# Performance work log

Measured on AMD Instinct MI355X. Metric: run time of the kernel, lower is better.

## Reference

```python
import jax, jax.numpy as jnp
import numpy as np

BATCH, FIELDS, DIM = 1024, 39, 32
L0_OUT, L1_OUT = 256, 128  # cin_layer_size


def setup_inputs() -> dict:
    key = jax.random.key(0)
    ks = jax.random.split(key, 5)
    x = jax.random.normal(ks[0], (BATCH, FIELDS, DIM), dtype=jnp.float32)
    # Conv1d(kernel_size=1) weights stored as (out_channels, in_channels)
    w0 = jax.random.normal(ks[1], (L0_OUT, FIELDS * FIELDS), dtype=jnp.float32) * 0.02
    b0 = jax.random.normal(ks[2], (L0_OUT,), dtype=jnp.float32) * 0.02
    w1 = jax.random.normal(ks[3], (L1_OUT, FIELDS * (L0_OUT // 2)), dtype=jnp.float32) * 0.02
    b1 = jax.random.normal(ks[4], (L1_OUT,), dtype=jnp.float32) * 0.02
    return {"x": x, "w0": w0, "b0": b0, "w1": w1, "b1": b1}


def _cin_layer(x0, h_prev, w, b):
    # outer product over field axes at each embedding position, then 1x1 conv (= GEMM over channels)
    bsz, m, d = x0.shape
    z = jnp.einsum('bmd,bnd->bmnd', x0, h_prev).reshape(bsz, m * h_prev.shape[1], d)
    return jax.nn.relu(jnp.einsum('bid,oi->bod', z, w) + b[None, :, None])


def reference(x, w0, b0, w1, b1):
    # Layer 0: cross x with itself -> (B, m*m, D) -> conv -> relu
    h0 = _cin_layer(x, x, w0, b0)            # (B, 256, D)
    h1a, h1b = jnp.split(h0, 2, axis=1)      # each (B, 128, D); h1a feeds next layer
    # Layer 1 (final): cross x with h1a
    h1 = _cin_layer(x, h1a, w1, b1)          # (B, 128, D)
    # sum-pool over embedding dim of concatenated hidden outputs (hidden_layer[1:])
    return jnp.sum(jnp.concatenate([h1b, h1], axis=1), axis=-1)  # (B, 256)
```

## Files before the change

### kernel.cpp

```cpp
#include <hip/hip_runtime.h>


typedef __bf16 bf16x8 __attribute__((ext_vector_type(8)));
typedef float f32x4 __attribute__((ext_vector_type(4)));

#define NB 2
#define NBLK 512
#define THREADS 256
#define K0STEPS 50

__global__ __launch_bounds__(256) void prep_kernel(
    const float* __restrict__ w0, const float* __restrict__ w1,
    __bf16* __restrict__ w0b, __bf16* __restrict__ w1p) {
  int stride = gridDim.x * blockDim.x;
  int tid = blockIdx.x * blockDim.x + threadIdx.x;
  const int n0 = K0STEPS * 256 * 32;
  for (int idx = tid; idx < n0; idx += stride) {
    int j = idx & 31, o = (idx >> 5) & 255, blk = idx >> 13;
    int ip = blk * 32 + j;
    float v = 0.f;
    if (ip < 1560) {
      unsigned m = (unsigned)ip / 40u;
      unsigned n = (unsigned)ip - m * 40u;
      if (n < 39u) v = w0[o * 1521 + m * 39 + n];
    }
    w0b[idx] = (__bf16)v;
  }
  const int n1 = 39 * 4 * 128 * 32;
  for (int idx = tid; idx < n1; idx += stride) {
    int j = idx & 31, o = (idx >> 5) & 127, q = idx >> 12;
    int ks = q & 3, m = q >> 2;
    w1p[idx] = (__bf16)w1[o * 4992 + m * 128 + ks * 32 + j];
  }
}

__global__ __launch_bounds__(256, 2) void cin_kernel(
    const float* __restrict__ x,
    const __bf16* __restrict__ w0b, const float* __restrict__ b0,
    const __bf16* __restrict__ w1p, const float* __restrict__ b1,
    float* __restrict__ out) {
  __shared__ __align__(16) __bf16 xs[NB * 32 * 40];
  __shared__ __align__(16) __bf16 zsm[2 * 64 * 32];
  __shared__ __align__(16) __bf16 h1[NB * 32 * 136];

  const int t = threadIdx.x;
  const int bb = blockIdx.x * NB;
  const int w = t >> 6;
  const int l15 = t & 15;
  const int lhi = (t >> 4) & 3;
  const int col = t & 63;
  const int kg = t >> 6;
  const int zwoff = col * 32 + ((kg ^ ((col >> 1) & 3)) * 8);

  for (int idx = t; idx < NB * 39 * 32; idx += THREADS) {
    int b = idx / 1248; int rem = idx - b * 1248;
    int m = rem >> 5; int d = rem & 31;
    xs[(b * 32 + d) * 40 + m] = (__bf16)x[(bb + b) * 1248 + rem];
  }
  if (t < NB * 32) xs[t * 40 + 39] = (__bf16)0.f;
  __syncthreads();

  int boff[4];
#pragma unroll
  for (int nt = 0; nt < 4; ++nt) {
    int cc = nt * 16 + l15;
    boff[nt] = cc * 32 + ((lhi ^ ((cc >> 1) & 3)) * 8);
  }

  f32x4 acc[4][4] = {};

  auto loadA0 = [&](int s, bf16x8 (&af)[4]) {
#pragma unroll
    for (int mt = 0; mt < 4; ++mt) {
      int o = w * 64 + mt * 16 + l15;
      af[mt] = *(const bf16x8*)(w0b + s * 8192 + o * 32 + lhi * 8);
    }
  };
  auto zgen0 = [&](int s, int buf) {
    int i0 = s * 32 + kg * 8;
    unsigned m = (unsigned)i0 / 40u;
    unsigned nb = (unsigned)i0 - m * 40u;
    float xm = (float)xs[col * 40 + m];
    bf16x8 xn = *(const bf16x8*)&xs[col * 40 + nb];
    bf16x8 vz;
#pragma unroll
    for (int jj = 0; jj < 8; ++jj) vz[jj] = (__bf16)(xm * (float)xn[jj]);
    *(bf16x8*)&zsm[buf * 2048 + zwoff] = vz;
  };
  auto compute0 = [&](int buf, bf16x8 (&af)[4]) {
    bf16x8 bfr[4];
#pragma unroll
    for (int nt = 0; nt < 4; ++nt) bfr[nt] = *(const bf16x8*)&zsm[buf * 2048 + boff[nt]];
#pragma unroll
    for (int mt = 0; mt < 4; ++mt)
#pragma unroll
      for (int nt = 0; nt < 4; ++nt)
        acc[mt][nt] = __builtin_amdgcn_mfma_f32_16x16x32_bf16(af[mt], bfr[nt], acc[mt][nt], 0, 0, 0);
  };

  bf16x8 afA[4], afB[4];
  loadA0(0, afA);
  zgen0(0, 0);
  __syncthreads();
  for (int s = 0; s < K0STEPS; s += 2) {
    loadA0(s + 1, afB);
    zgen0(s + 1, 1);
    compute0(0, afA);
    __syncthreads();
    if (s + 2 < K0STEPS) { loadA0(s + 2, afA); zgen0(s + 2, 0); }
    compute0(1, afB);
    __syncthreads();
  }

  if (w < 2) {
#pragma unroll
    for (int mt = 0; mt < 4; ++mt) {
#pragma unroll
      for (int nt = 0; nt < 4; ++nt) {
        int c = nt * 16 + l15;
        int hbase = c * 136;
#pragma unroll
        for (int r = 0; r < 4; ++r) {
          int o = w * 64 + mt * 16 + lhi * 4 + r;
          float v = fmaxf(acc[mt][nt][r] + b0[o], 0.f);
          h1[hbase + o] = (__bf16)v;
        }
      }
    }
  } else {
#pragma unroll
    for (int mt = 0; mt < 4; ++mt) {
#pragma unroll
      for (int r = 0; r < 4; ++r) {
        int o = w * 64 + mt * 16 + lhi * 4 + r;
        float bias = b0[o];
        float sb0 = 0.f, sb1 = 0.f;
#pragma unroll
        for (int nt = 0; nt < 4; ++nt) {
          float v = fmaxf(acc[mt][nt][r] + bias, 0.f);
          v += __shfl_xor(v, 1); v += __shfl_xor(v, 2);
          v += __shfl_xor(v, 4); v += __shfl_xor(v, 8);
          if (nt < 2) sb0 += v; else sb1 += v;
        }
        if (l15 == 0) {
          out[(bb + 0) * 256 + (o - 128)] = sb0;
          out[(bb + 1) * 256 + (o - 128)] = sb1;
        }
      }
    }
  }
  __syncthreads();

  bf16x8 hf[4][4];
#pragma unroll
  for (int ks = 0; ks < 4; ++ks)
#pragma unroll
    for (int nt = 0; nt < 4; ++nt)
      hf[ks][nt] = *(const bf16x8*)&h1[(nt * 16 + l15) * 136 + ks * 32 + lhi * 8];

  f32x4 acc2[2][4] = {};

  auto loadA1 = [&](int m, bf16x8 (&wf)[4][2]) {
#pragma unroll
    for (int ks = 0; ks < 4; ++ks)
#pragma unroll
      for (int mt = 0; mt < 2; ++mt) {
        int o = w * 32 + mt * 16 + l15;
        wf[ks][mt] = *(const bf16x8*)(w1p + ((m * 4 + ks) * 128 + o) * 32 + lhi * 8);
      }
  };
  auto computeM = [&](int m, bf16x8 (&wf)[4][2]) {
    float xmv[4];
#pragma unroll
    for (int nt = 0; nt < 4; ++nt) xmv[nt] = (float)xs[(nt * 16 + l15) * 40 + m];
    f32x4 Y[2][4];
#pragma unroll
    for (int ks = 0; ks < 4; ++ks)
#pragma unroll
      for (int mt = 0; mt < 2; ++mt)
#pragma unroll
        for (int nt = 0; nt < 4; ++nt) {
          f32x4 cin = (ks == 0) ? (f32x4){0.f, 0.f, 0.f, 0.f} : Y[mt][nt];
          Y[mt][nt] = __builtin_amdgcn_mfma_f32_16x16x32_bf16(wf[ks][mt], hf[ks][nt], cin, 0, 0, 0);
        }
#pragma unroll
    for (int mt = 0; mt < 2; ++mt)
#pragma unroll
      for (int nt = 0; nt < 4; ++nt)
#pragma unroll
        for (int r = 0; r < 4; ++r)
          acc2[mt][nt][r] += xmv[nt] * Y[mt][nt][r];
  };

  bf16x8 wfA[4][2], wfB[4][2];
  loadA1(0, wfA);
  loadA1(1, wfB);
  for (int m = 0; m < 38; m += 2) {
    computeM(m, wfA);
    if (m + 2 < 39) loadA1(m + 2, wfA);
    computeM(m + 1, wfB);
    if (m + 3 < 39) loadA1(m + 3, wfB);
  }
  computeM(38, wfA);

#pragma unroll
  for (int mt = 0; mt < 2; ++mt) {
#pragma unroll
    for (int r = 0; r < 4; ++r) {
      int o = w * 32 + mt * 16 + lhi * 4 + r;
      float bias = b1[o];
      float sb0 = 0.f, sb1 = 0.f;
#pragma unroll
      for (int nt = 0; nt < 4; ++nt) {
        float v = fmaxf(acc2[mt][nt][r] + bias, 0.f);
        v += __shfl_xor(v, 1); v += __shfl_xor(v, 2);
        v += __shfl_xor(v, 4); v += __shfl_xor(v, 8);
        if (nt < 2) sb0 += v; else sb1 += v;
      }
      if (l15 == 0) {
        out[(bb + 0) * 256 + 128 + o] = sb0;
        out[(bb + 1) * 256 + 128 + o] = sb1;
      }
    }
  }
}

extern "C" void kernel_launch(void* const* d_in, const int* in_sizes, int n_in,
                              void* d_out, int out_size, void* d_ws, size_t ws_size,
                              hipStream_t stream) {
  const float* x  = (const float*)d_in[0];
  const float* w0 = (const float*)d_in[1];
  const float* b0 = (const float*)d_in[2];
  const float* w1 = (const float*)d_in[3];
  const float* b1 = (const float*)d_in[4];
  float* out = (float*)d_out;

  __bf16* w0b = (__bf16*)d_ws;
  __bf16* w1p = w0b + K0STEPS * 256 * 32;

  prep_kernel<<<256, 256, 0, stream>>>(w0, w1, w0b, w1p);
  cin_kernel<<<NBLK, THREADS, 0, stream>>>(x, w0b, b0, w1p, b1, out);
}
```

Before: 104.7 us.

## Generate layer-0 Z fragments in registers per wave, dropping shared staging and barriers

Layer 0 of the CIN kernel no longer stages the outer-product Z tile in a double-buffered shared-memory array. Each wave now builds its own MFMA B fragments directly from xs in registers, which removes the per-step LDS writes and reads and both __syncthreads per iteration. The cost is that all four waves recompute the same Z values, roughly four times the conversion and multiply work per block. The division by 40 is also replaced with a multiply-shift, and the weight prefetch now runs two steps ahead.

```diff
diff --git a/kernel.cpp b/kernel.cpp
--- a/kernel.cpp
+++ b/kernel.cpp
@@ -40,7 +40,6 @@
     const __bf16* __restrict__ w1p, const float* __restrict__ b1,
     float* __restrict__ out) {
   __shared__ __align__(16) __bf16 xs[NB * 32 * 40];
-  __shared__ __align__(16) __bf16 zsm[2 * 64 * 32];
   __shared__ __align__(16) __bf16 h1[NB * 32 * 136];
 
   const int t = threadIdx.x;
@@ -48,9 +47,6 @@
   const int w = t >> 6;
   const int l15 = t & 15;
   const int lhi = (t >> 4) & 3;
-  const int col = t & 63;
-  const int kg = t >> 6;
-  const int zwoff = col * 32 + ((kg ^ ((col >> 1) & 3)) * 8);
 
   for (int idx = t; idx < NB * 39 * 32; idx += THREADS) {
     int b = idx / 1248; int rem = idx - b * 1248;
@@ -60,13 +56,6 @@
   if (t < NB * 32) xs[t * 40 + 39] = (__bf16)0.f;
   __syncthreads();
 
-  int boff[4];
-#pragma unroll
-  for (int nt = 0; nt < 4; ++nt) {
-    int cc = nt * 16 + l15;
-    boff[nt] = cc * 32 + ((lhi ^ ((cc >> 1) & 3)) * 8);
-  }
-
   f32x4 acc[4][4] = {};
 
   auto loadA0 = [&](int s, bf16x8 (&af)[4]) {
@@ -76,40 +65,40 @@
       af[mt] = *(const bf16x8*)(w0b + s * 8192 + o * 32 + lhi * 8);
     }
   };
-  auto zgen0 = [&](int s, int buf) {
-    int i0 = s * 32 + kg * 8;
-    unsigned m = (unsigned)i0 / 40u;
-    unsigned nb = (unsigned)i0 - m * 40u;
-    float xm = (float)xs[col * 40 + m];
-    bf16x8 xn = *(const bf16x8*)&xs[col * 40 + nb];
-    bf16x8 vz;
-#pragma unroll
-    for (int jj = 0; jj < 8; ++jj) vz[jj] = (__bf16)(xm * (float)xn[jj]);
-    *(bf16x8*)&zsm[buf * 2048 + zwoff] = vz;
-  };
-  auto compute0 = [&](int buf, bf16x8 (&af)[4]) {
-    bf16x8 bfr[4];
-#pragma unroll
-    for (int nt = 0; nt < 4; ++nt) bfr[nt] = *(const bf16x8*)&zsm[buf * 2048 + boff[nt]];
+  auto zfr = [&](int s, bf16x8 (&bz)[4]) {
+    unsigned i0 = (unsigned)(s * 32) + (unsigned)lhi * 8u;
+    unsigned m = (i0 * 52429u) >> 21;
+    unsigned nb = i0 - m * 40u;
+#pragma unroll
+    for (int nt = 0; nt < 4; ++nt) {
+      int c = nt * 16 + l15;
+      float xm = (float)xs[c * 40 + m];
+      bf16x8 xn = *(const bf16x8*)&xs[c * 40 + nb];
+      bf16x8 vz;
+#pragma unroll
+      for (int j = 0; j < 8; ++j) vz[j] = (__bf16)(xm * (float)xn[j]);
+      bz[nt] = vz;
+    }
+  };
+  auto comp0 = [&](bf16x8 (&af)[4], bf16x8 (&bz)[4]) {
 #pragma unroll
     for (int mt = 0; mt < 4; ++mt)
 #pragma unroll
       for (int nt = 0; nt < 4; ++nt)
-        acc[mt][nt] = __builtin_amdgcn_mfma_f32_16x16x32_bf16(af[mt], bfr[nt], acc[mt][nt], 0, 0, 0);
+        acc[mt][nt] = __builtin_amdgcn_mfma_f32_16x16x32_bf16(af[mt], bz[nt], acc[mt][nt], 0, 0, 0);
   };
 
   bf16x8 afA[4], afB[4];
   loadA0(0, afA);
-  zgen0(0, 0);
-  __syncthreads();
+  loadA0(1, afB);
   for (int s = 0; s < K0STEPS; s += 2) {
-    loadA0(s + 1, afB);
-    zgen0(s + 1, 1);
-    compute0(0, afA);
-    __syncthreads();
-    if (s + 2 < K0STEPS) { loadA0(s + 2, afA); zgen0(s + 2, 0); }
-    compute0(1, afB);
-    __syncthreads();
+    bf16x8 bzA[4], bzB[4];
+    zfr(s, bzA);
+    comp0(afA, bzA);
+    if (s + 2 < K0STEPS) loadA0(s + 2, afA);
+    zfr(s + 1, bzB);
+    comp0(afB, bzB);
+    if (s + 3 < K0STEPS) loadA0(s + 3, afB);
   }
 
   if (w < 2) {
```

Result: slower. 106.8 us (+2.1%).
